# Performance work log

Hardware: AMD Instinct MI355X
Metric: run time of the kernel (lower is better)

The kernel has to match this reference:

```python
import jax, jax.numpy as jnp
import numpy as np

NUM_HEADS = 8
HEAD_DIM = 64  # output_size
HIDDEN = 512
N_NODES = 4096


def setup_inputs() -> dict:
    key = jax.random.key(0)
    ks = jax.random.split(key, 9)
    s = 0.02
    return {
        "x": jax.random.normal(ks[0], (N_NODES, HIDDEN), dtype=jnp.float32),
        "Wq_w": jax.random.normal(ks[1], (HIDDEN, NUM_HEADS * HEAD_DIM), dtype=jnp.float32) * s,
        "Wq_b": jax.random.normal(ks[2], (NUM_HEADS * HEAD_DIM,), dtype=jnp.float32) * s,
        "Wk_w": jax.random.normal(ks[3], (HIDDEN, NUM_HEADS * HEAD_DIM), dtype=jnp.float32) * s,
        "Wk_b": jax.random.normal(ks[4], (NUM_HEADS * HEAD_DIM,), dtype=jnp.float32) * s,
        "Wv_w": jax.random.normal(ks[5], (HIDDEN, NUM_HEADS * HEAD_DIM), dtype=jnp.float32) * s,
        "Wv_b": jax.random.normal(ks[6], (NUM_HEADS * HEAD_DIM,), dtype=jnp.float32) * s,
        "Wo_w": jax.random.normal(ks[7], (NUM_HEADS * HEAD_DIM, HEAD_DIM), dtype=jnp.float32) * s,
        "Wo_b": jax.random.normal(ks[8], (HEAD_DIM,), dtype=jnp.float32) * s,
    }


def reference(x, Wq_w, Wq_b, Wk_w, Wk_b, Wv_w, Wv_b, Wo_w, Wo_b):
    N = x.shape[0]
    H, d = NUM_HEADS, HEAD_DIM
    # Projections: [N, H*d] -> [H, N, d]
    q = (x @ Wq_w + Wq_b).reshape(N, H, d).transpose(1, 0, 2)
    k = (x @ Wk_w + Wk_b).reshape(N, H, d).transpose(1, 0, 2)
    v = (x @ Wv_w + Wv_b).reshape(N, H, d).transpose(1, 0, 2)
    # Scaled dot-product attention per head: [H, N, N]
    scores = jnp.einsum('hnd,hmd->hnm', q, k) / jnp.sqrt(jnp.float32(d))
    attention_weights = jax.nn.softmax(scores, axis=-1)
    attended = jnp.einsum('hnm,hmd->hnd', attention_weights, v)  # [H, N, d]
    attended = attended.transpose(1, 0, 2).reshape(N, H * d)
    output = attended @ Wo_w + Wo_b  # [N, d]
    return output, attention_weights
```

## Files before the change

kernel.cpp:

```cpp
#include <hip/hip_runtime.h>

#define NN 4096
#define HID 512
#define NH 8
#define HD 64

typedef __attribute__((ext_vector_type(8))) short short8;
typedef __attribute__((ext_vector_type(4))) float f32x4;

__device__ __forceinline__ ushort f2bf(float f) {
    unsigned u = __float_as_uint(f);
    return (ushort)((u + 0x7FFFu + ((u >> 16) & 1u)) >> 16);
}
__device__ __forceinline__ float bf2f(ushort h) {
    return __uint_as_float((unsigned)h << 16);
}

__device__ __forceinline__ void gld16(const void* g, void* l) {
    __builtin_amdgcn_global_load_lds(
        (const __attribute__((address_space(1))) void*)g,
        (__attribute__((address_space(3))) void*)l, 16, 0, 0);
}

__global__ __launch_bounds__(256) void cvt_x_kernel(
    const float* __restrict__ x, ushort* __restrict__ xh, ushort* __restrict__ xl)
{
    int i = (blockIdx.x * 256 + threadIdx.x) * 8;
    float4 v0 = *(const float4*)(x + i);
    float4 v1 = *(const float4*)(x + i + 4);
    float v[8] = {v0.x, v0.y, v0.z, v0.w, v1.x, v1.y, v1.z, v1.w};
    ushort h[8], l[8];
#pragma unroll
    for (int j = 0; j < 8; ++j) {
        h[j] = f2bf(v[j]);
        l[j] = f2bf(v[j] - bf2f(h[j]));
    }
    ushort4 u;
    u.x = h[0]; u.y = h[1]; u.z = h[2]; u.w = h[3]; *(ushort4*)(xh + i) = u;
    u.x = h[4]; u.y = h[5]; u.z = h[6]; u.w = h[7]; *(ushort4*)(xh + i + 4) = u;
    u.x = l[0]; u.y = l[1]; u.z = l[2]; u.w = l[3]; *(ushort4*)(xl + i) = u;
    u.x = l[4]; u.y = l[5]; u.z = l[6]; u.w = l[7]; *(ushort4*)(xl + i + 4) = u;
}

__global__ __launch_bounds__(256) void cvt_w_kernel(
    const float* __restrict__ Wq, const float* __restrict__ Wk,
    const float* __restrict__ Wv,
    ushort* __restrict__ Wph, ushort* __restrict__ Wpl)
{
    const int mat = blockIdx.z;
    const float* W = (mat == 0) ? Wq : ((mat == 1) ? Wk : Wv);
    const int col = blockIdx.x * 256 + threadIdx.x;
    const int kcb = blockIdx.y;
    ushort* dh = Wph + (size_t)mat * 262144 + kcb * 16384 + col * 32;
    ushort* dl = Wpl + (size_t)mat * 262144 + kcb * 16384 + col * 32;
#pragma unroll
    for (int k4 = 0; k4 < 8; ++k4) {
        ushort4 uh, ul;
#pragma unroll
        for (int j = 0; j < 4; ++j) {
            float v = W[(size_t)(kcb * 32 + k4 * 4 + j) * HID + col];
            ushort h = f2bf(v);
            (&uh.x)[j] = h;
            (&ul.x)[j] = f2bf(v - bf2f(h));
        }
        *(ushort4*)(dh + k4 * 4) = uh;
        *(ushort4*)(dl + k4 * 4) = ul;
    }
}

__global__ __launch_bounds__(256) void qkv_mfma_kernel(
    const ushort* __restrict__ xh, const ushort* __restrict__ xl,
    const ushort* __restrict__ Wph, const ushort* __restrict__ Wpl,
    const float* __restrict__ bq, const float* __restrict__ bk,
    const float* __restrict__ bv,
    ushort* __restrict__ Qb, char* __restrict__ Kbs, char* __restrict__ Vts)
{
    const int mat = blockIdx.z;
    const int row0 = blockIdx.y * 128;
    const int col0 = blockIdx.x * 64;
    const int tid = threadIdx.x;
    const int w = tid >> 6, lane = tid & 63, g = lane >> 4, li = lane & 15;
    const ushort* Bh = Wph + (size_t)mat * 262144;
    const ushort* Bl = Wpl + (size_t)mat * 262144;
    const float* bias = (mat == 0) ? bq : ((mat == 1) ? bk : bv);

    __shared__ __align__(16) char smem[18432];

    f32x4 acc[2][4];
#pragma unroll
    for (int sb = 0; sb < 2; ++sb)
#pragma unroll
        for (int cf = 0; cf < 4; ++cf) acc[sb][cf] = (f32x4){0.f, 0.f, 0.f, 0.f};

    const ushort* xr0h = xh + (size_t)(row0 + w * 32 + li) * HID;
    const ushort* xr1h = xr0h + 16 * HID;
    const ushort* xr0l = xl + (size_t)(row0 + w * 32 + li) * HID;
    const ushort* xr1l = xr0l + 16 * HID;

#pragma unroll 2
    for (int kcb = 0; kcb < 16; ++kcb) {
        const int ko = kcb * 32 + g * 8;
        short8 a0h = *(const short8*)(xr0h + ko);
        short8 a1h = *(const short8*)(xr1h + ko);
        short8 a0l = *(const short8*)(xr0l + ko);
        short8 a1l = *(const short8*)(xr1l + ko);
        const ushort* bbh = Bh + kcb * 16384 + (col0 + li) * 32 + g * 8;
        const ushort* bbl = Bl + kcb * 16384 + (col0 + li) * 32 + g * 8;
#pragma unroll
        for (int cf = 0; cf < 4; ++cf) {
            short8 bhf = *(const short8*)(bbh + cf * 512);
            short8 blf = *(const short8*)(bbl + cf * 512);
            acc[0][cf] = __builtin_amdgcn_mfma_f32_16x16x32_bf16(a0l, bhf, acc[0][cf], 0, 0, 0);
            acc[0][cf] = __builtin_amdgcn_mfma_f32_16x16x32_bf16(a0h, blf, acc[0][cf], 0, 0, 0);
            acc[0][cf] = __builtin_amdgcn_mfma_f32_16x16x32_bf16(a0h, bhf, acc[0][cf], 0, 0, 0);
            acc[1][cf] = __builtin_amdgcn_mfma_f32_16x16x32_bf16(a1l, bhf, acc[1][cf], 0, 0, 0);
            acc[1][cf] = __builtin_amdgcn_mfma_f32_16x16x32_bf16(a1h, blf, acc[1][cf], 0, 0, 0);
            acc[1][cf] = __builtin_amdgcn_mfma_f32_16x16x32_bf16(a1h, bhf, acc[1][cf], 0, 0, 0);
        }
    }

    float bv_f[4];
#pragma unroll
    for (int cf = 0; cf < 4; ++cf) bv_f[cf] = bias[col0 + cf * 16 + li];

    const int head = col0 >> 6;
    if (mat < 2) {
        ushort* st = (ushort*)smem;
#pragma unroll
        for (int sb = 0; sb < 2; ++sb)
#pragma unroll
            for (int cf = 0; cf < 4; ++cf)
#pragma unroll
                for (int r = 0; r < 4; ++r)
                    st[(w * 32 + sb * 16 + g * 4 + r) * 72 + cf * 16 + li] =
                        f2bf(acc[sb][cf][r] + bv_f[cf]);
        __syncthreads();
        int row = tid >> 1, hf = tid & 1;
        const ushort* src = st + row * 72 + hf * 32;
        if (mat == 0) {
            ushort* dst = Qb + ((size_t)head * NN + row0 + row) * HD + hf * 32;
#pragma unroll
            for (int c = 0; c < 4; ++c)
                *(uint4*)(dst + c * 8) = *(const uint4*)(src + c * 8);
        } else {
            char* dst = Kbs + ((size_t)head * NN + row0 + row) * 128;
#pragma unroll
            for (int j8 = 0; j8 < 4; ++j8) {
                int j = hf * 4 + j8;
                *(uint4*)(dst + ((j * 16) ^ ((row & 7) << 4))) =
                    *(const uint4*)(st + row * 72 + j * 8);
            }
        }
    } else {
        ushort* vst = (ushort*)smem;
#pragma unroll
        for (int sb = 0; sb < 2; ++sb)
#pragma unroll
            for (int cf = 0; cf < 4; ++cf) {
                ushort4 pk;
                pk.x = f2bf(acc[sb][cf][0] + bv_f[cf]);
                pk.y = f2bf(acc[sb][cf][1] + bv_f[cf]);
                pk.z = f2bf(acc[sb][cf][2] + bv_f[cf]);
                pk.w = f2bf(acc[sb][cf][3] + bv_f[cf]);
                *(ushort4*)(vst + (cf * 16 + li) * 136 + w * 32 + sb * 16 + g * 4) = pk;
            }
        __syncthreads();
        int cl = tid >> 2, q = tid & 3;
        int dsw = (cl & 7) << 4;
        char* dstrow = Vts + (size_t)(col0 + cl) * (NN * 2);
        int colb0 = (row0 + q * 32) * 2;
#pragma unroll
        for (int k8 = 0; k8 < 4; ++k8)
            *(uint4*)(dstrow + ((colb0 + k8 * 16) ^ dsw)) =
                *(const uint4*)(vst + cl * 136 + q * 32 + k8 * 8);
    }
}

__global__ __launch_bounds__(512, 4) void attn_kernel(
    const ushort* __restrict__ Qb, const char* __restrict__ Kbs,
    const char* __restrict__ Vts,
    float* __restrict__ wout, float* __restrict__ att)
{
    const int h = blockIdx.x & 7;
    const int row0 = ((blockIdx.x >> 3) + (blockIdx.y << 3)) * 64;
    const int tid = threadIdx.x;
    const int w = tid >> 6, lane = tid & 63;
    const int g = lane >> 4, li = lane & 15;
    const int rgrp = w >> 1, khalf = w & 1;
    const int qr = row0 + rgrp * 16;

    const ushort* Qh = Qb + (size_t)h * NN * HD;
    const char* Kh = Kbs + (size_t)h * NN * 128;
    const char* Vh = Vts + (size_t)h * HD * NN * 2;
    float* WH = wout + ((size_t)h << 24);

    __shared__ __align__(16) char smem[81920];
    char* kbuf0 = smem;
    char* kbuf1 = smem + 16384;
    char* vbuf0 = smem + 32768;
    char* vbuf1 = smem + 49152;
    char* pbuf  = smem + 65536;
    float* zpart = (float*)(smem + 65536);
    float* attstage = (float*)(smem + 65536);

    const short8 qa0 = *(const short8*)(Qh + (size_t)(qr + li) * HD + g * 8);
    const short8 qa1 = *(const short8*)(Qh + (size_t)(qr + li) * HD + 32 + g * 8);
    const int sw = (li & 7) << 4;

    const int kl0 = w * 16 + (lane >> 3);
    const int kbase0 = (kl0 & 63) + ((kl0 >= 64) ? 2048 : 0);
    const int kl1 = kl0 + 8;
    const int kbase1 = (kl1 & 63) + ((kl1 >= 64) ? 2048 : 0);
    const size_t koff0 = (size_t)kbase0 * 128 + (lane & 7) * 16;
    const size_t koff1 = (size_t)kbase1 * 128 + (lane & 7) * 16;
    const int vd0 = w * 8 + (lane >> 4);
    const int vd1 = vd0 + 4;
    const size_t voff0 = (size_t)vd0 * 8192 + ((lane >> 3) & 1) * 4096 + (lane & 7) * 16;
    const size_t voff1 = (size_t)vd1 * 8192 + ((lane >> 3) & 1) * 4096 + (lane & 7) * 16;
    const int ldst = w * 2048 + lane * 16;

    float zsum = 0.f;
    {
        char* c0 = kbuf0; char* c1 = kbuf1; char* c2 = vbuf0;
        gld16(Kh + koff0, c0 + ldst);
        gld16(Kh + koff1, c0 + ldst + 1024);
        gld16(Kh + 8192 + koff0, c1 + ldst);
        gld16(Kh + 8192 + koff1, c1 + ldst + 1024);
        asm volatile("" ::: "memory");
        for (int t = 0; t < 32; ++t) {
            if (t < 31) { asm volatile("s_waitcnt vmcnt(2)" ::: "memory"); }
            else        { asm volatile("s_waitcnt vmcnt(0)" ::: "memory"); }
            __builtin_amdgcn_s_barrier();
            if (t + 2 < 32) {
                gld16(Kh + (size_t)(t + 2) * 8192 + koff0, c2 + ldst);
                gld16(Kh + (size_t)(t + 2) * 8192 + koff1, c2 + ldst + 1024);
            }
            asm volatile("" ::: "memory");
#pragma unroll
            for (int jt = 0; jt < 4; ++jt) {
                const char* rp = c0 + (khalf * 64 + jt * 16 + li) * 128;
                short8 kb0 = *(const short8*)(rp + ((g * 16) ^ sw));
                short8 kb1 = *(const short8*)(rp + ((64 + g * 16) ^ sw));
                f32x4 acc = {0.f, 0.f, 0.f, 0.f};
                acc = __builtin_amdgcn_mfma_f32_16x16x32_bf16(kb0, qa0, acc, 0, 0, 0);
                acc = __builtin_amdgcn_mfma_f32_16x16x32_bf16(kb1, qa1, acc, 0, 0, 0);
#pragma unroll
                for (int r = 0; r < 4; ++r) zsum += __expf(acc[r] * 0.125f);
            }
            char* tmp = c0; c0 = c1; c1 = c2; c2 = tmp;
        }
    }
    zsum += __shfl_xor(zsum, 16);
    zsum += __shfl_xor(zsum, 32);
    if (lane < 16) zpart[w * 16 + li] = zsum;
    __syncthreads();
    const float iz = 1.0f / (zpart[(rgrp * 2) * 16 + li] + zpart[(rgrp * 2 + 1) * 16 + li]);
    __syncthreads();

    f32x4 pv[4];
#pragma unroll
    for (int dt = 0; dt < 4; ++dt) pv[dt] = (f32x4){0.f, 0.f, 0.f, 0.f};
    char* myp = pbuf + w * 2048;

    {
        char* kc = kbuf0; char* kn = kbuf1;
        char* vc = vbuf0; char* vn = vbuf1;
        gld16(Kh + koff0, kc + ldst);
        gld16(Kh + koff1, kc + ldst + 1024);
        gld16(Vh + voff0, vc + ldst);
        gld16(Vh + voff1, vc + ldst + 1024);
        asm volatile("" ::: "memory");
        for (int t = 0; t < 32; ++t) {
            if (t == 0) { asm volatile("s_waitcnt vmcnt(0)" ::: "memory"); }
            else        { asm volatile("s_waitcnt vmcnt(4)" ::: "memory"); }
            __builtin_amdgcn_s_barrier();
            if (t + 1 < 32) {
                gld16(Kh + (size_t)(t + 1) * 8192 + koff0, kn + ldst);
                gld16(Kh + (size_t)(t + 1) * 8192 + koff1, kn + ldst + 1024);
                gld16(Vh + (size_t)(t + 1) * 128 + voff0, vn + ldst);
                gld16(Vh + (size_t)(t + 1) * 128 + voff1, vn + ldst + 1024);
            }
            asm volatile("" ::: "memory");
#pragma unroll
            for (int jt = 0; jt < 4; ++jt) {
                const char* rp = kc + (khalf * 64 + jt * 16 + li) * 128;
                short8 kb0 = *(const short8*)(rp + ((g * 16) ^ sw));
                short8 kb1 = *(const short8*)(rp + ((64 + g * 16) ^ sw));
                f32x4 acc = {0.f, 0.f, 0.f, 0.f};
                acc = __builtin_amdgcn_mfma_f32_16x16x32_bf16(kb0, qa0, acc, 0, 0, 0);
                acc = __builtin_amdgcn_mfma_f32_16x16x32_bf16(kb1, qa1, acc, 0, 0, 0);
                f32x4 ev;
#pragma unroll
                for (int r = 0; r < 4; ++r) ev[r] = __expf(acc[r] * 0.125f) * iz;
                *(f32x4*)(WH + (size_t)(qr + li) * NN + khalf * 2048 + t * 64 + jt * 16 + g * 4) = ev;
                uint pk0 = (uint)f2bf(ev[0]) | ((uint)f2bf(ev[1]) << 16);
                uint pk1 = (uint)f2bf(ev[2]) | ((uint)f2bf(ev[3]) << 16);
                int boff = (li * 128 + jt * 32 + g * 8) ^ sw;
                *(uint2*)(myp + boff) = make_uint2(pk0, pk1);
            }
#pragma unroll
            for (int kb2 = 0; kb2 < 2; ++kb2) {
                int rbp = (li * 128 + kb2 * 64 + g * 16) ^ sw;
                short8 pa = *(const short8*)(myp + rbp);
#pragma unroll
                for (int dt = 0; dt < 4; ++dt) {
                    const char* vrp = vc + (dt * 16 + li) * 256 + khalf * 128;
                    short8 vbf = *(const short8*)(vrp + ((kb2 * 64 + g * 16) ^ sw));
                    pv[dt] = __builtin_amdgcn_mfma_f32_16x16x32_bf16(pa, vbf, pv[dt], 0, 0, 0);
                }
            }
            char* tmp = kc; kc = kn; kn = tmp;
            tmp = vc; vc = vn; vn = tmp;
        }
    }

    __syncthreads();
    if (khalf == 1) {
#pragma unroll
        for (int dt = 0; dt < 4; ++dt)
#pragma unroll
            for (int r = 0; r < 4; ++r)
                attstage[(rgrp * 16 + g * 4 + r) * 64 + dt * 16 + li] = pv[dt][r];
    }
    __syncthreads();
    if (khalf == 0) {
#pragma unroll
        for (int dt = 0; dt < 4; ++dt)
#pragma unroll
            for (int r = 0; r < 4; ++r) {
                float v = pv[dt][r] + attstage[(rgrp * 16 + g * 4 + r) * 64 + dt * 16 + li];
                att[(size_t)(qr + g * 4 + r) * HID + h * HD + dt * 16 + li] = v;
            }
    }
}

__global__ __launch_bounds__(256) void out_kernel(
    const float* __restrict__ att, const float* __restrict__ Wo,
    const float* __restrict__ bo, float* __restrict__ outp)
{
    const int row0 = blockIdx.x * 16;
    const int tid = threadIdx.x;
    const int tx = tid & 15, ty = tid >> 4;

    __shared__ float as_[64][20];
    __shared__ float ws2[64][68];

    float acc[4] = {0.f, 0.f, 0.f, 0.f};

    for (int kc = 0; kc < HID; kc += 64) {
        {
            int i = tid >> 4, k4 = tid & 15;
            float4 v = *(const float4*)(att + (size_t)(row0 + i) * HID + kc + k4 * 4);
            as_[k4 * 4 + 0][i] = v.x; as_[k4 * 4 + 1][i] = v.y;
            as_[k4 * 4 + 2][i] = v.z; as_[k4 * 4 + 3][i] = v.w;
        }
#pragma unroll
        for (int it = 0; it < 4; ++it) {
            int f = it * 256 + tid;
            int k = f >> 4, c4 = f & 15;
            float4 v = *(const float4*)(Wo + (size_t)(kc + k) * HD + c4 * 4);
            *(float4*)&ws2[k][c4 * 4] = v;
        }
        __syncthreads();
        for (int k = 0; k < 64; ++k) {
            float a = as_[k][ty];
            float4 b0 = *(const float4*)&ws2[k][tx * 4];
            acc[0] = fmaf(a, b0.x, acc[0]);
            acc[1] = fmaf(a, b0.y, acc[1]);
            acc[2] = fmaf(a, b0.z, acc[2]);
            acc[3] = fmaf(a, b0.w, acc[3]);
        }
        __syncthreads();
    }

    float4 v;
    v.x = acc[0] + bo[tx * 4 + 0];
    v.y = acc[1] + bo[tx * 4 + 1];
    v.z = acc[2] + bo[tx * 4 + 2];
    v.w = acc[3] + bo[tx * 4 + 3];
    *(float4*)(outp + (size_t)(row0 + ty) * HD + tx * 4) = v;
}

extern "C" void kernel_launch(void* const* d_in, const int* in_sizes, int n_in,
                              void* d_out, int out_size, void* d_ws, size_t ws_size,
                              hipStream_t stream) {
    const float* x  = (const float*)d_in[0];
    const float* Wq = (const float*)d_in[1];
    const float* bq = (const float*)d_in[2];
    const float* Wk = (const float*)d_in[3];
    const float* bk = (const float*)d_in[4];
    const float* Wv = (const float*)d_in[5];
    const float* bv = (const float*)d_in[6];
    const float* Wo = (const float*)d_in[7];
    const float* bo = (const float*)d_in[8];

    float* out  = (float*)d_out;
    float* wout = out + (size_t)NN * HD;

    char* wsb = (char*)d_ws;
    ushort* Qb  = (ushort*)wsb;
    char*   Kbs = wsb + 4u * 1024u * 1024u;
    char*   Vts = wsb + 8u * 1024u * 1024u;
    float*  att = (float*)(wsb + 12u * 1024u * 1024u);
    ushort* xh  = (ushort*)(wsb + 20u * 1024u * 1024u);
    ushort* xl  = (ushort*)(wsb + 24u * 1024u * 1024u);
    ushort* Wph = (ushort*)(wsb + 28u * 1024u * 1024u);
    ushort* Wpl = (ushort*)(wsb + 30u * 1024u * 1024u);

    hipLaunchKernelGGL(cvt_x_kernel, dim3(1024), dim3(256), 0, stream, x, xh, xl);
    hipLaunchKernelGGL(cvt_w_kernel, dim3(2, 16, 3), dim3(256), 0, stream,
                       Wq, Wk, Wv, Wph, Wpl);
    hipLaunchKernelGGL(qkv_mfma_kernel, dim3(8, 32, 3), dim3(256), 0, stream,
                       xh, xl, Wph, Wpl, bq, bk, bv, Qb, Kbs, Vts);
    hipLaunchKernelGGL(attn_kernel, dim3(64, NH), dim3(512), 0, stream,
                       Qb, Kbs, Vts, wout, att);
    hipLaunchKernelGGL(out_kernel, dim3(256), dim3(256), 0, stream,
                       att, Wo, bo, out);
}
```

Baseline: 246.3 us.

## Split softmax normalizer pass into separate z-pass and reduction kernels

Moves the first pass of the attention kernel, which computes the softmax denominator over all 4096 keys, into its own kernel. That kernel runs 2048 blocks of 16 query rows, with each wave covering a quarter of the keys and reading K straight from global memory into registers with a software prefetch. A small reduction kernel sums the four partials and stores 1/Z, which the weight pass then reads. The goal is more parallelism and freeing the main kernel's LDS pipeline, at the cost of two extra launches and rereading K from global/L2 without LDS sharing.

```diff
diff --git a/kernel.cpp b/kernel.cpp
--- a/kernel.cpp
+++ b/kernel.cpp
@@ -176,9 +176,71 @@
     }
 }
 
-__global__ __launch_bounds__(512, 4) void attn_kernel(
+__device__ __forceinline__ void prefks(short8 (&K)[8], const char* __restrict__ Kh,
+                                       int bb, int li, int g, int sw) {
+#pragma unroll
+    for (int jj = 0; jj < 4; ++jj) {
+        const char* rp = Kh + (size_t)(bb + jj * 16 + li) * 128;
+        K[jj * 2 + 0] = *(const short8*)(rp + ((g * 16) ^ sw));
+        K[jj * 2 + 1] = *(const short8*)(rp + ((64 + g * 16) ^ sw));
+    }
+}
+
+__device__ __forceinline__ void bodyAz(const short8 (&K)[8], short8 qa0, short8 qa1,
+                                       float& zsum) {
+#pragma unroll
+    for (int jj = 0; jj < 4; ++jj) {
+        f32x4 acc = {0.f, 0.f, 0.f, 0.f};
+        acc = __builtin_amdgcn_mfma_f32_16x16x32_bf16(K[jj * 2 + 0], qa0, acc, 0, 0, 0);
+        acc = __builtin_amdgcn_mfma_f32_16x16x32_bf16(K[jj * 2 + 1], qa1, acc, 0, 0, 0);
+#pragma unroll
+        for (int r = 0; r < 4; ++r) zsum += __expf(acc[r] * 0.125f);
+    }
+}
+
+__global__ __launch_bounds__(256) void zpass_kernel(
     const ushort* __restrict__ Qb, const char* __restrict__ Kbs,
-    const char* __restrict__ Vts,
+    float* __restrict__ Zp)
+{
+    const int bid = blockIdx.x;
+    const int h = bid & 7;
+    const int qr = (bid >> 3) * 16;
+    const int tid = threadIdx.x;
+    const int w = tid >> 6, lane = tid & 63, g = lane >> 4, li = lane & 15;
+    const ushort* Qh = Qb + (size_t)h * NN * HD;
+    const char* Kh = Kbs + (size_t)h * NN * 128;
+    const int sw = (li & 7) << 4;
+
+    const short8 qa0 = *(const short8*)(Qh + (size_t)(qr + li) * HD + g * 8);
+    const short8 qa1 = *(const short8*)(Qh + (size_t)(qr + li) * HD + 32 + g * 8);
+
+    const int k0 = w * 1024;
+    short8 kA[8], kB[8];
+    float zsum = 0.f;
+    prefks(kA, Kh, k0, li, g, sw);
+    for (int c = 0; c < 16; c += 2) {
+        prefks(kB, Kh, k0 + (c + 1) * 64, li, g, sw);
+        bodyAz(kA, qa0, qa1, zsum);
+        if (c + 2 < 16) prefks(kA, Kh, k0 + (c + 2) * 64, li, g, sw);
+        bodyAz(kB, qa0, qa1, zsum);
+    }
+    zsum += __shfl_xor(zsum, 16);
+    zsum += __shfl_xor(zsum, 32);
+    if (lane < 16)
+        Zp[((size_t)h * NN + qr + li) * 4 + w] = zsum;
+}
+
+__global__ __launch_bounds__(256) void zred_kernel(
+    const float* __restrict__ Zp, float* __restrict__ invZ)
+{
+    int idx = blockIdx.x * 256 + threadIdx.x;
+    f32x4 v = *(const f32x4*)(Zp + (size_t)idx * 4);
+    invZ[idx] = 1.0f / (v[0] + v[1] + v[2] + v[3]);
+}
+
+__global__ __launch_bounds__(512, 4) void wpass_kernel(
+    const ushort* __restrict__ Qb, const char* __restrict__ Kbs,
+    const char* __restrict__ Vts, const float* __restrict__ invZ,
     float* __restrict__ wout, float* __restrict__ att)
 {
     const int h = blockIdx.x & 7;
@@ -200,12 +262,12 @@
     char* vbuf0 = smem + 32768;
     char* vbuf1 = smem + 49152;
     char* pbuf  = smem + 65536;
-    float* zpart = (float*)(smem + 65536);
     float* attstage = (float*)(smem + 65536);
 
     const short8 qa0 = *(const short8*)(Qh + (size_t)(qr + li) * HD + g * 8);
     const short8 qa1 = *(const short8*)(Qh + (size_t)(qr + li) * HD + 32 + g * 8);
     const int sw = (li & 7) << 4;
+    const float iz = invZ[(size_t)h * NN + qr + li];
 
     const int kl0 = w * 16 + (lane >> 3);
     const int kbase0 = (kl0 & 63) + ((kl0 >= 64) ? 2048 : 0);
@@ -218,44 +280,6 @@
     const size_t voff0 = (size_t)vd0 * 8192 + ((lane >> 3) & 1) * 4096 + (lane & 7) * 16;
     const size_t voff1 = (size_t)vd1 * 8192 + ((lane >> 3) & 1) * 4096 + (lane & 7) * 16;
     const int ldst = w * 2048 + lane * 16;
-
-    float zsum = 0.f;
-    {
-        char* c0 = kbuf0; char* c1 = kbuf1; char* c2 = vbuf0;
-        gld16(Kh + koff0, c0 + ldst);
-        gld16(Kh + koff1, c0 + ldst + 1024);
-        gld16(Kh + 8192 + koff0, c1 + ldst);
-        gld16(Kh + 8192 + koff1, c1 + ldst + 1024);
-        asm volatile("" ::: "memory");
-        for (int t = 0; t < 32; ++t) {
-            if (t < 31) { asm volatile("s_waitcnt vmcnt(2)" ::: "memory"); }
-            else        { asm volatile("s_waitcnt vmcnt(0)" ::: "memory"); }
-            __builtin_amdgcn_s_barrier();
-            if (t + 2 < 32) {
-                gld16(Kh + (size_t)(t + 2) * 8192 + koff0, c2 + ldst);
-                gld16(Kh + (size_t)(t + 2) * 8192 + koff1, c2 + ldst + 1024);
-            }
-            asm volatile("" ::: "memory");
-#pragma unroll
-            for (int jt = 0; jt < 4; ++jt) {
-                const char* rp = c0 + (khalf * 64 + jt * 16 + li) * 128;
-                short8 kb0 = *(const short8*)(rp + ((g * 16) ^ sw));
-                short8 kb1 = *(const short8*)(rp + ((64 + g * 16) ^ sw));
-                f32x4 acc = {0.f, 0.f, 0.f, 0.f};
-                acc = __builtin_amdgcn_mfma_f32_16x16x32_bf16(kb0, qa0, acc, 0, 0, 0);
-                acc = __builtin_amdgcn_mfma_f32_16x16x32_bf16(kb1, qa1, acc, 0, 0, 0);
-#pragma unroll
-                for (int r = 0; r < 4; ++r) zsum += __expf(acc[r] * 0.125f);
-            }
-            char* tmp = c0; c0 = c1; c1 = c2; c2 = tmp;
-        }
-    }
-    zsum += __shfl_xor(zsum, 16);
-    zsum += __shfl_xor(zsum, 32);
-    if (lane < 16) zpart[w * 16 + li] = zsum;
-    __syncthreads();
-    const float iz = 1.0f / (zpart[(rgrp * 2) * 16 + li] + zpart[(rgrp * 2 + 1) * 16 + li]);
-    __syncthreads();
 
     f32x4 pv[4];
 #pragma unroll
@@ -406,14 +430,20 @@
     ushort* xl  = (ushort*)(wsb + 24u * 1024u * 1024u);
     ushort* Wph = (ushort*)(wsb + 28u * 1024u * 1024u);
     ushort* Wpl = (ushort*)(wsb + 30u * 1024u * 1024u);
+    float*  Zp   = (float*)(wsb + 32u * 1024u * 1024u);
+    float*  invZ = (float*)(wsb + 33u * 1024u * 1024u);
 
     hipLaunchKernelGGL(cvt_x_kernel, dim3(1024), dim3(256), 0, stream, x, xh, xl);
     hipLaunchKernelGGL(cvt_w_kernel, dim3(2, 16, 3), dim3(256), 0, stream,
                        Wq, Wk, Wv, Wph, Wpl);
     hipLaunchKernelGGL(qkv_mfma_kernel, dim3(8, 32, 3), dim3(256), 0, stream,
                        xh, xl, Wph, Wpl, bq, bk, bv, Qb, Kbs, Vts);
-    hipLaunchKernelGGL(attn_kernel, dim3(64, NH), dim3(512), 0, stream,
-                       Qb, Kbs, Vts, wout, att);
+    hipLaunchKernelGGL(zpass_kernel, dim3(2048), dim3(256), 0, stream,
+                       Qb, Kbs, Zp);
+    hipLaunchKernelGGL(zred_kernel, dim3(128), dim3(256), 0, stream,
+                       Zp, invZ);
+    hipLaunchKernelGGL(wpass_kernel, dim3(64, NH), dim3(512), 0, stream,
+                       Qb, Kbs, Vts, invZ, wout, att);
     hipLaunchKernelGGL(out_kernel, dim3(256), dim3(256), 0, stream,
                        att, Wo, bo, out);
 }
```

Result: slower. 281.7 us (+14.4%).

## Halve attention block to 32 query rows with smaller K/V tiles

Applied to the files above, without the earlier changes.

Shrinks the attention block from 512 to 256 threads, covering 32 query rows with 32-key tiles per half, and launches 1024 blocks instead of 512. Shared memory is halved, and the V tile load and indexing are rewritten with a new swizzle for the narrower tile. The goal is more resident blocks per CU, better latency hiding and finer load balance. The cost is that each block streams all of K and V for fewer query rows, which doubles the total K/V traffic, and twice as many loop iterations means more barriers.

```diff
diff --git a/kernel.cpp b/kernel.cpp
--- a/kernel.cpp
+++ b/kernel.cpp
@@ -176,13 +176,14 @@
     }
 }
 
-__global__ __launch_bounds__(512, 4) void attn_kernel(
+__global__ __launch_bounds__(256, 4) void attn_kernel(
     const ushort* __restrict__ Qb, const char* __restrict__ Kbs,
     const char* __restrict__ Vts,
     float* __restrict__ wout, float* __restrict__ att)
 {
-    const int h = blockIdx.x & 7;
-    const int row0 = ((blockIdx.x >> 3) + (blockIdx.y << 3)) * 64;
+    const int bid = blockIdx.x;
+    const int h = bid & 7;
+    const int row0 = (bid >> 3) * 32;
     const int tid = threadIdx.x;
     const int w = tid >> 6, lane = tid & 63;
     const int g = lane >> 4, li = lane & 15;
@@ -194,51 +195,48 @@
     const char* Vh = Vts + (size_t)h * HD * NN * 2;
     float* WH = wout + ((size_t)h << 24);
 
-    __shared__ __align__(16) char smem[81920];
+    __shared__ __align__(16) char smem[40960];
     char* kbuf0 = smem;
-    char* kbuf1 = smem + 16384;
-    char* vbuf0 = smem + 32768;
-    char* vbuf1 = smem + 49152;
-    char* pbuf  = smem + 65536;
-    float* zpart = (float*)(smem + 65536);
-    float* attstage = (float*)(smem + 65536);
+    char* kbuf1 = smem + 8192;
+    char* vbuf0 = smem + 16384;
+    char* vbuf1 = smem + 24576;
+    char* pbuf  = smem + 32768;
+    float* zpart = (float*)(smem + 32768);
+    float* attstage = (float*)(smem + 32768);
 
     const short8 qa0 = *(const short8*)(Qh + (size_t)(qr + li) * HD + g * 8);
     const short8 qa1 = *(const short8*)(Qh + (size_t)(qr + li) * HD + 32 + g * 8);
     const int sw = (li & 7) << 4;
 
-    const int kl0 = w * 16 + (lane >> 3);
-    const int kbase0 = (kl0 & 63) + ((kl0 >= 64) ? 2048 : 0);
-    const int kl1 = kl0 + 8;
-    const int kbase1 = (kl1 & 63) + ((kl1 >= 64) ? 2048 : 0);
-    const size_t koff0 = (size_t)kbase0 * 128 + (lane & 7) * 16;
-    const size_t koff1 = (size_t)kbase1 * 128 + (lane & 7) * 16;
-    const int vd0 = w * 8 + (lane >> 4);
-    const int vd1 = vd0 + 4;
-    const size_t voff0 = (size_t)vd0 * 8192 + ((lane >> 3) & 1) * 4096 + (lane & 7) * 16;
-    const size_t voff1 = (size_t)vd1 * 8192 + ((lane >> 3) & 1) * 4096 + (lane & 7) * 16;
-    const int ldst = w * 2048 + lane * 16;
+    const int r0 = w * 8 + (lane >> 3);
+    const int inb = (lane & 7) * 16;
+    const int L0 = w * 1024 + lane * 16;
+    const int d0 = r0;
+    const int hs = (lane & 7) ^ (d0 & 7);
+    const int vh = hs >> 2, vs = hs & 3;
+    const int vdsw = d0 & 7;
+    const int vro = (((khalf << 2) | g) ^ (li & 7)) << 4;
 
     float zsum = 0.f;
     {
         char* c0 = kbuf0; char* c1 = kbuf1; char* c2 = vbuf0;
-        gld16(Kh + koff0, c0 + ldst);
-        gld16(Kh + koff1, c0 + ldst + 1024);
-        gld16(Kh + 8192 + koff0, c1 + ldst);
-        gld16(Kh + 8192 + koff1, c1 + ldst + 1024);
+        gld16(Kh + (size_t)(r0) * 128 + inb, c0 + L0);
+        gld16(Kh + (size_t)(2048 + r0) * 128 + inb, c0 + L0 + 4096);
+        gld16(Kh + (size_t)(r0 + 32) * 128 + inb, c1 + L0);
+        gld16(Kh + (size_t)(2048 + r0 + 32) * 128 + inb, c1 + L0 + 4096);
         asm volatile("" ::: "memory");
-        for (int t = 0; t < 32; ++t) {
-            if (t < 31) { asm volatile("s_waitcnt vmcnt(2)" ::: "memory"); }
+        for (int t = 0; t < 64; ++t) {
+            if (t < 63) { asm volatile("s_waitcnt vmcnt(2)" ::: "memory"); }
             else        { asm volatile("s_waitcnt vmcnt(0)" ::: "memory"); }
             __builtin_amdgcn_s_barrier();
-            if (t + 2 < 32) {
-                gld16(Kh + (size_t)(t + 2) * 8192 + koff0, c2 + ldst);
-                gld16(Kh + (size_t)(t + 2) * 8192 + koff1, c2 + ldst + 1024);
+            if (t + 2 < 64) {
+                gld16(Kh + (size_t)(r0 + (t + 2) * 32) * 128 + inb, c2 + L0);
+                gld16(Kh + (size_t)(2048 + r0 + (t + 2) * 32) * 128 + inb, c2 + L0 + 4096);
             }
             asm volatile("" ::: "memory");
 #pragma unroll
-            for (int jt = 0; jt < 4; ++jt) {
-                const char* rp = c0 + (khalf * 64 + jt * 16 + li) * 128;
+            for (int jt = 0; jt < 2; ++jt) {
+                const char* rp = c0 + (khalf * 32 + jt * 16 + li) * 128;
                 short8 kb0 = *(const short8*)(rp + ((g * 16) ^ sw));
                 short8 kb1 = *(const short8*)(rp + ((64 + g * 16) ^ sw));
                 f32x4 acc = {0.f, 0.f, 0.f, 0.f};
@@ -265,25 +263,31 @@
     {
         char* kc = kbuf0; char* kn = kbuf1;
         char* vc = vbuf0; char* vn = vbuf1;
-        gld16(Kh + koff0, kc + ldst);
-        gld16(Kh + koff1, kc + ldst + 1024);
-        gld16(Vh + voff0, vc + ldst);
-        gld16(Vh + voff1, vc + ldst + 1024);
+        gld16(Kh + (size_t)(r0) * 128 + inb, kc + L0);
+        gld16(Kh + (size_t)(2048 + r0) * 128 + inb, kc + L0 + 4096);
+        {
+            size_t tail0 = (size_t)vh * 4096 + (((((0 & 1) << 2) | vs) ^ vdsw) << 4);
+            gld16(Vh + (size_t)d0 * 8192 + tail0, vc + L0);
+            gld16(Vh + (size_t)(d0 + 32) * 8192 + tail0, vc + L0 + 4096);
+        }
         asm volatile("" ::: "memory");
-        for (int t = 0; t < 32; ++t) {
+        for (int t = 0; t < 64; ++t) {
             if (t == 0) { asm volatile("s_waitcnt vmcnt(0)" ::: "memory"); }
-            else        { asm volatile("s_waitcnt vmcnt(4)" ::: "memory"); }
+            else        { asm volatile("s_waitcnt vmcnt(2)" ::: "memory"); }
             __builtin_amdgcn_s_barrier();
-            if (t + 1 < 32) {
-                gld16(Kh + (size_t)(t + 1) * 8192 + koff0, kn + ldst);
-                gld16(Kh + (size_t)(t + 1) * 8192 + koff1, kn + ldst + 1024);
-                gld16(Vh + (size_t)(t + 1) * 128 + voff0, vn + ldst);
-                gld16(Vh + (size_t)(t + 1) * 128 + voff1, vn + ldst + 1024);
+            if (t + 1 < 64) {
+                int tn = t + 1;
+                gld16(Kh + (size_t)(r0 + tn * 32) * 128 + inb, kn + L0);
+                gld16(Kh + (size_t)(2048 + r0 + tn * 32) * 128 + inb, kn + L0 + 4096);
+                size_t tail = (size_t)vh * 4096 + (size_t)(tn >> 1) * 128
+                            + ((((tn & 1) << 2 | vs) ^ vdsw) << 4);
+                gld16(Vh + (size_t)d0 * 8192 + tail, vn + L0);
+                gld16(Vh + (size_t)(d0 + 32) * 8192 + tail, vn + L0 + 4096);
             }
             asm volatile("" ::: "memory");
 #pragma unroll
-            for (int jt = 0; jt < 4; ++jt) {
-                const char* rp = kc + (khalf * 64 + jt * 16 + li) * 128;
+            for (int jt = 0; jt < 2; ++jt) {
+                const char* rp = kc + (khalf * 32 + jt * 16 + li) * 128;
                 short8 kb0 = *(const short8*)(rp + ((g * 16) ^ sw));
                 short8 kb1 = *(const short8*)(rp + ((64 + g * 16) ^ sw));
                 f32x4 acc = {0.f, 0.f, 0.f, 0.f};
@@ -292,20 +296,19 @@
                 f32x4 ev;
 #pragma unroll
                 for (int r = 0; r < 4; ++r) ev[r] = __expf(acc[r] * 0.125f) * iz;
-                *(f32x4*)(WH + (size_t)(qr + li) * NN + khalf * 2048 + t * 64 + jt * 16 + g * 4) = ev;
+                *(f32x4*)(WH + (size_t)(qr + li) * NN + khalf * 2048 + t * 32 + jt * 16 + g * 4) = ev;
                 uint pk0 = (uint)f2bf(ev[0]) | ((uint)f2bf(ev[1]) << 16);
                 uint pk1 = (uint)f2bf(ev[2]) | ((uint)f2bf(ev[3]) << 16);
                 int boff = (li * 128 + jt * 32 + g * 8) ^ sw;
                 *(uint2*)(myp + boff) = make_uint2(pk0, pk1);
             }
-#pragma unroll
-            for (int kb2 = 0; kb2 < 2; ++kb2) {
-                int rbp = (li * 128 + kb2 * 64 + g * 16) ^ sw;
+            {
+                int rbp = (li * 128 + g * 16) ^ sw;
                 short8 pa = *(const short8*)(myp + rbp);
 #pragma unroll
                 for (int dt = 0; dt < 4; ++dt) {
-                    const char* vrp = vc + (dt * 16 + li) * 256 + khalf * 128;
-                    short8 vbf = *(const short8*)(vrp + ((kb2 * 64 + g * 16) ^ sw));
+                    const char* vrp = vc + (dt * 16 + li) * 128 + vro;
+                    short8 vbf = *(const short8*)(vrp);
                     pv[dt] = __builtin_amdgcn_mfma_f32_16x16x32_bf16(pa, vbf, pv[dt], 0, 0, 0);
                 }
             }
@@ -412,7 +415,7 @@
                        Wq, Wk, Wv, Wph, Wpl);
     hipLaunchKernelGGL(qkv_mfma_kernel, dim3(8, 32, 3), dim3(256), 0, stream,
                        xh, xl, Wph, Wpl, bq, bk, bv, Qb, Kbs, Vts);
-    hipLaunchKernelGGL(attn_kernel, dim3(64, NH), dim3(512), 0, stream,
+    hipLaunchKernelGGL(attn_kernel, dim3(1024), dim3(256), 0, stream,
                        Qb, Kbs, Vts, wout, att);
     hipLaunchKernelGGL(out_kernel, dim3(256), dim3(256), 0, stream,
                        att, Wo, bo, out);
```

New measurement: 236.9 us. 3.8% less time.
